# Optimization experiments

Hardware: AMD Instinct MI355X
Metric: run time of the kernel (lower is better)

## Reference

```python
import jax, jax.numpy as jnp
import numpy as np

N = 50000
L = 3


def gcn_conv(x, W, b, src, dst):
    """PyG-style GCNConv: add self-loops, symmetric deg^-1/2 normalization,
    linear transform, scatter-add aggregation at destination nodes."""
    loops = jnp.arange(N, dtype=src.dtype)
    s = jnp.concatenate([src, loops])  # [E+N]
    d = jnp.concatenate([dst, loops])
    deg = jax.ops.segment_sum(jnp.ones(s.shape[0], x.dtype), d, num_segments=N)
    dinv = jnp.where(deg > 0, jax.lax.rsqrt(deg), jnp.zeros_like(deg))
    norm = dinv[s] * dinv[d]  # [E+N]
    xw = x @ W  # [N, F_out]
    out = jax.ops.segment_sum(xw[s] * norm[:, None], d, num_segments=N)
    return out + b


def setup_inputs() -> dict:
    key = jax.random.key(0)
    ks = jax.random.split(key, 6)
    E = 1600000
    F_in, F_hid, F_out = 256, 128, 64
    x = jax.random.normal(ks[0], (N, F_in), dtype=jnp.float32)
    edges = jax.random.randint(ks[1], (L, 2, E), 0, N, dtype=jnp.int32)
    W1 = jax.random.normal(ks[2], (L, F_in, F_hid), dtype=jnp.float32) * (1.0 / np.sqrt(F_in))
    b1 = jnp.zeros((L, F_hid), dtype=jnp.float32)
    W2 = jax.random.normal(ks[3], (L, F_hid, F_out), dtype=jnp.float32) * (1.0 / np.sqrt(F_hid))
    b2 = jnp.zeros((L, F_out), dtype=jnp.float32)
    return {"x": x, "edges": edges, "W1": W1, "b1": b1, "W2": W2, "b2": b2}


def reference(x, edges, W1, b1, W2, b2):
    # layer 1: sum of L GCNConvs over the L rewired graphs
    h = jnp.zeros((N, W1.shape[2]), dtype=x.dtype)
    for i in range(L):
        h = h + gcn_conv(x, W1[i], b1[i], edges[i, 0], edges[i, 1])
    h = jax.nn.relu(h)
    # layer 2
    out = jnp.zeros((N, W2.shape[2]), dtype=x.dtype)
    for i in range(L):
        out = out + gcn_conv(h, W2[i], b2[i], edges[i, 0], edges[i, 1])
    return out
```

## Files before the change

kernel.cpp:

```cpp
#include <hip/hip_runtime.h>

typedef unsigned int uint;
typedef unsigned short ushort;

#define NN 50000
#define NE 1600000
#define NL 3
#define NB 782
#define CAP 2560
#define CHUNK 8192

typedef float f32x4 __attribute__((ext_vector_type(4)));
typedef __bf16 bf16x4v __attribute__((ext_vector_type(4)));
typedef __bf16 bf16x8v __attribute__((ext_vector_type(8)));

__device__ __forceinline__ ushort f2bf(float f) {
    uint u = __float_as_uint(f);
    u += 0x7fffu + ((u >> 16) & 1u);
    return (ushort)(u >> 16);
}
__device__ __forceinline__ float bf2f(uint lo16) { return __uint_as_float(lo16 << 16); }

__global__ void zero_k(int* __restrict__ p, int n) {
    int i = blockIdx.x * 256 + threadIdx.x;
    if (i < n) p[i] = 0;
}

__global__ void cvt_x(const float4* __restrict__ x, ushort4* __restrict__ xb) {
    int idx = blockIdx.x * 256 + threadIdx.x;
    float4 v = x[idx];
    ushort4 o;
    o.x = f2bf(v.x); o.y = f2bf(v.y); o.z = f2bf(v.z); o.w = f2bf(v.w);
    xb[idx] = o;
}

__global__ void cvt_w(const float* __restrict__ W1, const float* __restrict__ W2,
                      ushort* __restrict__ w1t, ushort* __restrict__ w2t) {
    int idx = blockIdx.x * 256 + threadIdx.x;
    const int n1 = NL * 256 * 128;
    const int n2 = NL * 128 * 64;
    if (idx < n1) {
        int i = idx / (128 * 256);
        int rem = idx % (128 * 256);
        int c = rem / 256, k = rem % 256;
        w1t[idx] = f2bf(W1[i * 256 * 128 + k * 128 + c]);
    } else if (idx < n1 + n2) {
        int j = idx - n1;
        int i = j / (64 * 128);
        int rem = j % (64 * 128);
        int c = rem / 128, k = rem % 128;
        w2t[j] = f2bf(W2[i * 128 * 64 + k * 64 + c]);
    }
}

__global__ __launch_bounds__(256) void bin_edges(const int* __restrict__ edges,
                                                 int* __restrict__ gcur,
                                                 uint* __restrict__ bins) {
    __shared__ uint hist[NB];
    __shared__ uint base[NB];
    const int t = threadIdx.x;
    const int g = blockIdx.y;
    const int e0 = blockIdx.x * CHUNK;
    const int n = min(CHUNK, NE - e0);
    const int* srcp = edges + (size_t)g * 2 * NE;
    const int* dstp = srcp + NE;

    for (int b = t; b < NB; b += 256) hist[b] = 0u;
    __syncthreads();
    for (int k = t; k < n; k += 256) {
        int dst = dstp[e0 + k];
        atomicAdd(&hist[dst >> 6], 1u);
    }
    __syncthreads();
    for (int b = t; b < NB; b += 256) {
        uint cnt = hist[b];
        base[b] = cnt ? (uint)atomicAdd(&gcur[g * NB + b], (int)cnt) : 0u;
        hist[b] = 0u;
    }
    __syncthreads();
    for (int k = t; k < n; k += 256) {
        int dst = dstp[e0 + k];
        int src = srcp[e0 + k];
        int b = dst >> 6;
        uint r = atomicAdd(&hist[b], 1u);
        bins[((size_t)g * NB + b) * CAP + base[b] + r] = ((uint)(dst & 63) << 16) | (uint)src;
    }
}

__global__ __launch_bounds__(256) void csr_bucket(const uint* __restrict__ bins,
                                                  const int* __restrict__ gcur,
                                                  uint* __restrict__ rowse,
                                                  float* __restrict__ dinv,
                                                  ushort* __restrict__ colv16) {
    __shared__ uint h[64];
    __shared__ uint off[64];
    const int t = threadIdx.x;
    const int b = blockIdx.x;
    const int g = blockIdx.y;
    if (t < 64) h[t] = 0u;
    __syncthreads();
    const int n = gcur[g * NB + b];
    const uint* pe = bins + ((size_t)g * NB + b) * CAP;
    for (int k = t; k < n; k += 256) atomicAdd(&h[pe[k] >> 16], 1u);
    __syncthreads();
    if (t < 64) {
        uint cnt = h[t];
        uint x = cnt;
#pragma unroll
        for (int o = 1; o < 64; o <<= 1) {
            uint y = __shfl_up(x, o, 64);
            if (t >= o) x += y;
        }
        uint excl = x - cnt;
        off[t] = excl;
        int v = b * 64 + t;
        if (v < NN) {
            rowse[g * NN + v] = (uint)(b * CAP) + excl | (cnt << 24);
            dinv[g * NN + v] = rsqrtf((float)(cnt + 1));
        }
    }
    __syncthreads();
    if (t < 64) h[t] = off[t];
    __syncthreads();
    ushort* cp = colv16 + (size_t)g * NB * CAP + (size_t)b * CAP;
    for (int k = t; k < n; k += 256) {
        uint e = pe[k];
        uint pos = atomicAdd(&h[e >> 16], 1u);
        cp[pos] = (ushort)(e & 0xffffu);
    }
}

template <int KTOT, int BN, bool QUANT>
__global__ __launch_bounds__(256) void gemm_scaled(const ushort* __restrict__ A,
                                                   const ushort* __restrict__ Bt,
                                                   const float* __restrict__ dinv,
                                                   ushort* __restrict__ OutBf,
                                                   char* __restrict__ OutQ,
                                                   float* __restrict__ OutSc, int M) {
    constexpr int LDT = 72;
    constexpr int NREP = BN / 32;
    __shared__ ushort sA[128 * LDT];
    __shared__ ushort sB[BN * LDT];
    __shared__ float pmax[128][2];
    const int t = threadIdx.x;
    const int lane = t & 63;
    const int wid = t >> 6;
    const int wm = wid >> 1, wn = wid & 1;
    const int by = blockIdx.y;
    const int m0 = blockIdx.x * 128;
    const int sr = t >> 3, sc = t & 7;
    const int lr = lane & 15, lg = lane >> 4;

    f32x4 acc[4][NREP];
#pragma unroll
    for (int m = 0; m < 4; ++m)
#pragma unroll
        for (int n = 0; n < NREP; ++n) acc[m][n] = (f32x4){0.f, 0.f, 0.f, 0.f};

    for (int ks = 0; ks < KTOT / 64; ++ks) {
        __syncthreads();
#pragma unroll
        for (int p = 0; p < 4; ++p) {
            int r = sr + p * 32;
            int grow = m0 + r;
            uint4 val = make_uint4(0u, 0u, 0u, 0u);
            if (grow < M)
                val = *reinterpret_cast<const uint4*>(&A[(size_t)grow * KTOT + ks * 64 + sc * 8]);
            *reinterpret_cast<uint4*>(&sA[r * LDT + sc * 8]) = val;
        }
#pragma unroll
        for (int p = 0; p < BN / 32; ++p) {
            int r = sr + p * 32;
            uint4 val =
                *reinterpret_cast<const uint4*>(&Bt[(size_t)(by * BN + r) * KTOT + ks * 64 + sc * 8]);
            *reinterpret_cast<uint4*>(&sB[r * LDT + sc * 8]) = val;
        }
        __syncthreads();
#pragma unroll
        for (int kk = 0; kk < 2; ++kk) {
            const int kb = kk * 32 + lg * 4;
            bf16x8v af[4], bfr[NREP];
#pragma unroll
            for (int m = 0; m < 4; ++m) {
                const __bf16* p =
                    reinterpret_cast<const __bf16*>(&sA[(wm * 64 + m * 16 + lr) * LDT + kb]);
                bf16x4v lo = *reinterpret_cast<const bf16x4v*>(p);
                bf16x4v hi = *reinterpret_cast<const bf16x4v*>(p + 16);
                af[m] = __builtin_shufflevector(lo, hi, 0, 1, 2, 3, 4, 5, 6, 7);
            }
#pragma unroll
            for (int n = 0; n < NREP; ++n) {
                const __bf16* p =
                    reinterpret_cast<const __bf16*>(&sB[(wn * (BN / 2) + n * 16 + lr) * LDT + kb]);
                bf16x4v lo = *reinterpret_cast<const bf16x4v*>(p);
                bf16x4v hi = *reinterpret_cast<const bf16x4v*>(p + 16);
                bfr[n] = __builtin_shufflevector(lo, hi, 0, 1, 2, 3, 4, 5, 6, 7);
            }
#pragma unroll
            for (int m = 0; m < 4; ++m)
#pragma unroll
                for (int n = 0; n < NREP; ++n)
                    acc[m][n] =
                        __builtin_amdgcn_mfma_f32_16x16x32_bf16(af[m], bfr[n], acc[m][n], 0, 0, 0);
        }
    }
    if constexpr (!QUANT) {
#pragma unroll
        for (int m = 0; m < 4; ++m) {
            int rb = m0 + wm * 64 + m * 16 + lg * 4;
#pragma unroll
            for (int n = 0; n < NREP; ++n) {
                int lcol = wn * (BN / 2) + n * 16 + lr;
#pragma unroll
                for (int r = 0; r < 4; ++r) {
                    int grow = rb + r;
                    if (grow < M) {
                        float v = acc[m][n][r] * dinv[by * NN + grow];
                        OutBf[((size_t)by * M + grow) * BN + lcol] = f2bf(v);
                    }
                }
            }
        }
    } else {
        float pm[4][4];
#pragma unroll
        for (int m = 0; m < 4; ++m)
#pragma unroll
            for (int r = 0; r < 4; ++r) {
                float v = fabsf(acc[m][0][r]);
#pragma unroll
                for (int n = 1; n < NREP; ++n) v = fmaxf(v, fabsf(acc[m][n][r]));
#pragma unroll
                for (int o = 1; o < 16; o <<= 1) v = fmaxf(v, __shfl_xor(v, o, 64));
                pm[m][r] = v;
            }
        if (lr == 0) {
#pragma unroll
            for (int m = 0; m < 4; ++m)
#pragma unroll
                for (int r = 0; r < 4; ++r) pmax[wm * 64 + m * 16 + lg * 4 + r][wn] = pm[m][r];
        }
        __syncthreads();
#pragma unroll
        for (int m = 0; m < 4; ++m) {
#pragma unroll
            for (int r = 0; r < 4; ++r) {
                int brow = wm * 64 + m * 16 + lg * 4 + r;
                int grow = m0 + brow;
                if (grow >= M) continue;
                float mx = fmaxf(pmax[brow][0], pmax[brow][1]);
                float rs = (mx > 0.f) ? 127.f / mx : 0.f;
#pragma unroll
                for (int n = 0; n < NREP; ++n) {
                    int q = (int)rintf(acc[m][n][r] * rs);
                    OutQ[((size_t)by * NN + grow) * BN + wn * 64 + n * 16 + lr] = (char)q;
                }
                if (wn == 0 && lr == 0)
                    OutSc[by * NN + grow] =
                        (mx > 0.f) ? mx * dinv[by * NN + grow] * (1.f / 127.f) : 0.f;
            }
        }
    }
}

__global__ __launch_bounds__(256) void agg_l1(const ushort* __restrict__ q1,
                                              const float* __restrict__ q1sc,
                                              const ushort* __restrict__ colv16,
                                              const uint* __restrict__ rowse,
                                              const float* __restrict__ b1,
                                              ushort* __restrict__ hout) {
    const int lane = threadIdx.x & 63;
    const int v = blockIdx.x * 4 + (threadIdx.x >> 6);
    float h0 = 0.f, h1 = 0.f;
#pragma unroll
    for (int i = 0; i < NL; ++i) {
        const ushort* tab = q1 + (size_t)i * NN * 64;
        const float* scp = q1sc + i * NN;
        const ushort* cp = colv16 + (size_t)i * NB * CAP;
        uint se = rowse[i * NN + v];
        int e = (int)(se & 0xffffffu);
        int cnt = (int)(se >> 24);
        const int end = e + cnt;
        float dv = rsqrtf((float)(cnt + 1));
        ushort su = tab[(size_t)v * 64 + lane];
        float ssc = scp[v];
        float a0 = ssc * (float)(char)(su & 0xff);
        float a1 = ssc * (float)(char)(su >> 8);
        for (; e + 8 <= end; e += 8) {
            int s0 = cp[e], s1 = cp[e + 1], s2 = cp[e + 2], s3 = cp[e + 3];
            int s4 = cp[e + 4], s5 = cp[e + 5], s6 = cp[e + 6], s7 = cp[e + 7];
            ushort u0 = tab[(size_t)s0 * 64 + lane];
            ushort u1 = tab[(size_t)s1 * 64 + lane];
            ushort u2 = tab[(size_t)s2 * 64 + lane];
            ushort u3 = tab[(size_t)s3 * 64 + lane];
            ushort u4 = tab[(size_t)s4 * 64 + lane];
            ushort u5 = tab[(size_t)s5 * 64 + lane];
            ushort u6 = tab[(size_t)s6 * 64 + lane];
            ushort u7 = tab[(size_t)s7 * 64 + lane];
            float c0 = scp[s0], c1 = scp[s1], c2 = scp[s2], c3 = scp[s3];
            float c4 = scp[s4], c5 = scp[s5], c6 = scp[s6], c7 = scp[s7];
            a0 = fmaf(c0, (float)(char)(u0 & 0xff), a0); a1 = fmaf(c0, (float)(char)(u0 >> 8), a1);
            a0 = fmaf(c1, (float)(char)(u1 & 0xff), a0); a1 = fmaf(c1, (float)(char)(u1 >> 8), a1);
            a0 = fmaf(c2, (float)(char)(u2 & 0xff), a0); a1 = fmaf(c2, (float)(char)(u2 >> 8), a1);
            a0 = fmaf(c3, (float)(char)(u3 & 0xff), a0); a1 = fmaf(c3, (float)(char)(u3 >> 8), a1);
            a0 = fmaf(c4, (float)(char)(u4 & 0xff), a0); a1 = fmaf(c4, (float)(char)(u4 >> 8), a1);
            a0 = fmaf(c5, (float)(char)(u5 & 0xff), a0); a1 = fmaf(c5, (float)(char)(u5 >> 8), a1);
            a0 = fmaf(c6, (float)(char)(u6 & 0xff), a0); a1 = fmaf(c6, (float)(char)(u6 >> 8), a1);
            a0 = fmaf(c7, (float)(char)(u7 & 0xff), a0); a1 = fmaf(c7, (float)(char)(u7 >> 8), a1);
        }
        for (; e < end; ++e) {
            int s = cp[e];
            ushort u = tab[(size_t)s * 64 + lane];
            float c = scp[s];
            a0 = fmaf(c, (float)(char)(u & 0xff), a0);
            a1 = fmaf(c, (float)(char)(u >> 8), a1);
        }
        h0 = fmaf(dv, a0, h0);
        h1 = fmaf(dv, a1, h1);
    }
    int f0 = lane * 2;
    h0 += b1[f0] + b1[128 + f0] + b1[256 + f0];
    h1 += b1[f0 + 1] + b1[128 + f0 + 1] + b1[256 + f0 + 1];
    h0 = fmaxf(h0, 0.f);
    h1 = fmaxf(h1, 0.f);
    uint o = (uint)f2bf(h0) | ((uint)f2bf(h1) << 16);
    reinterpret_cast<uint*>(hout)[(size_t)v * 64 + lane] = o;
}

__global__ __launch_bounds__(256) void agg_l2(const ushort* __restrict__ hw2s,
                                              const ushort* __restrict__ colv16,
                                              const uint* __restrict__ rowse,
                                              const float* __restrict__ b2,
                                              float* __restrict__ out) {
    const int lane = threadIdx.x & 63;
    const int v = blockIdx.x * 4 + (threadIdx.x >> 6);
    float o = 0.f;
#pragma unroll
    for (int i = 0; i < NL; ++i) {
        const ushort* tab = hw2s + (size_t)i * NN * 64;
        const ushort* cp = colv16 + (size_t)i * NB * CAP;
        uint se = rowse[i * NN + v];
        int e = (int)(se & 0xffffffu);
        int cnt = (int)(se >> 24);
        const int end = e + cnt;
        float dv = rsqrtf((float)(cnt + 1));
        float a = bf2f(tab[(size_t)v * 64 + lane]);
        for (; e + 8 <= end; e += 8) {
            int s0 = cp[e], s1 = cp[e + 1], s2 = cp[e + 2], s3 = cp[e + 3];
            int s4 = cp[e + 4], s5 = cp[e + 5], s6 = cp[e + 6], s7 = cp[e + 7];
            float x0 = bf2f(tab[(size_t)s0 * 64 + lane]);
            float x1 = bf2f(tab[(size_t)s1 * 64 + lane]);
            float x2 = bf2f(tab[(size_t)s2 * 64 + lane]);
            float x3 = bf2f(tab[(size_t)s3 * 64 + lane]);
            float x4 = bf2f(tab[(size_t)s4 * 64 + lane]);
            float x5 = bf2f(tab[(size_t)s5 * 64 + lane]);
            float x6 = bf2f(tab[(size_t)s6 * 64 + lane]);
            float x7 = bf2f(tab[(size_t)s7 * 64 + lane]);
            a += ((x0 + x1) + (x2 + x3)) + ((x4 + x5) + (x6 + x7));
        }
        for (; e < end; ++e) a += bf2f(tab[(size_t)cp[e] * 64 + lane]);
        o = fmaf(dv, a, o);
    }
    o += b2[lane] + b2[64 + lane] + b2[128 + lane];
    out[(size_t)v * 64 + lane] = o;
}

extern "C" void kernel_launch(void* const* d_in, const int* in_sizes, int n_in,
                              void* d_out, int out_size, void* d_ws, size_t ws_size,
                              hipStream_t stream) {
    const float* x = (const float*)d_in[0];
    const int* edges = (const int*)d_in[1];
    const float* W1 = (const float*)d_in[2];
    const float* b1 = (const float*)d_in[3];
    const float* W2 = (const float*)d_in[4];
    const float* b2 = (const float*)d_in[5];
    float* out = (float*)d_out;
    char* ws = (char*)d_ws;

    ushort* xbf    = (ushort*)(ws + 0);
    ushort* w1t    = (ushort*)(ws + 25600000);
    ushort* w2t    = (ushort*)(ws + 25796608);
    uint*   rowse  = (uint*)  (ws + 25845760);
    float*  q1sc   = (float*) (ws + 26445760);
    float*  dinv   = (float*) (ws + 27045760);
    int*    gcur   = (int*)   (ws + 27645760);
    ushort* colv16 = (ushort*)(ws + 27655168);
    uint*   bins   = (uint*)  (ws + 39666688);
    char*   q1     = (char*)  (ws + 63689728);
    ushort* hbf    = (ushort*)(ws + 82889728);
    ushort* hw2s   = (ushort*)(ws + 95689728);

    zero_k<<<dim3((NL * NB + 255) / 256), 256, 0, stream>>>(gcur, NL * NB);
    cvt_x<<<dim3(12500), 256, 0, stream>>>((const float4*)x, (ushort4*)xbf);
    cvt_w<<<dim3(480), 256, 0, stream>>>(W1, W2, w1t, w2t);

    bin_edges<<<dim3((NE + CHUNK - 1) / CHUNK, NL), 256, 0, stream>>>(edges, gcur, bins);
    csr_bucket<<<dim3(NB, NL), 256, 0, stream>>>(bins, gcur, rowse, dinv, colv16);

    gemm_scaled<256, 128, true><<<dim3(391, 3), 256, 0, stream>>>(xbf, w1t, dinv, nullptr, q1,
                                                                  q1sc, NN);
    agg_l1<<<dim3(NN / 4), 256, 0, stream>>>((const ushort*)q1, q1sc, colv16, rowse, b1, hbf);
    gemm_scaled<128, 64, false><<<dim3(391, 3), 256, 0, stream>>>(hbf, w2t, dinv, hw2s, nullptr,
                                                                  nullptr, NN);
    agg_l2<<<dim3(NN / 4), 256, 0, stream>>>(hw2s, colv16, rowse, b2, out);
}
```

Baseline: 435.1 us.

## Fuse fp32-to-bf16 conversion of x into layer-1 GEMM load; nontemporal index loads

Drops the standalone x conversion kernel and converts fp32 x to bf16 inside the first GEMM's shared-memory tile load. This removes a launch and the round trip of the bf16 copy of x through memory. The trade-off is that each of the three column blocks rereads the fp32 x, doubling the bytes per read. The CSR column-index loads in both aggregation kernels now use nontemporal loads to reduce cache pollution.

```diff
diff --git a/kernel.cpp b/kernel.cpp
--- a/kernel.cpp
+++ b/kernel.cpp
@@ -24,14 +24,6 @@
 __global__ void zero_k(int* __restrict__ p, int n) {
     int i = blockIdx.x * 256 + threadIdx.x;
     if (i < n) p[i] = 0;
-}
-
-__global__ void cvt_x(const float4* __restrict__ x, ushort4* __restrict__ xb) {
-    int idx = blockIdx.x * 256 + threadIdx.x;
-    float4 v = x[idx];
-    ushort4 o;
-    o.x = f2bf(v.x); o.y = f2bf(v.y); o.z = f2bf(v.z); o.w = f2bf(v.w);
-    xb[idx] = o;
 }
 
 __global__ void cvt_w(const float* __restrict__ W1, const float* __restrict__ W2,
@@ -130,8 +122,8 @@
     }
 }
 
-template <int KTOT, int BN, bool QUANT>
-__global__ __launch_bounds__(256) void gemm_scaled(const ushort* __restrict__ A,
+template <int KTOT, int BN, bool QUANT, bool F32A>
+__global__ __launch_bounds__(256) void gemm_scaled(const void* __restrict__ Ap,
                                                    const ushort* __restrict__ Bt,
                                                    const float* __restrict__ dinv,
                                                    ushort* __restrict__ OutBf,
@@ -164,8 +156,22 @@
             int r = sr + p * 32;
             int grow = m0 + r;
             uint4 val = make_uint4(0u, 0u, 0u, 0u);
-            if (grow < M)
-                val = *reinterpret_cast<const uint4*>(&A[(size_t)grow * KTOT + ks * 64 + sc * 8]);
+            if (grow < M) {
+                if constexpr (F32A) {
+                    const float* Af = (const float*)Ap;
+                    const float4 lo4 =
+                        *reinterpret_cast<const float4*>(&Af[(size_t)grow * KTOT + ks * 64 + sc * 8]);
+                    const float4 hi4 = *reinterpret_cast<const float4*>(
+                        &Af[(size_t)grow * KTOT + ks * 64 + sc * 8 + 4]);
+                    val.x = (uint)f2bf(lo4.x) | ((uint)f2bf(lo4.y) << 16);
+                    val.y = (uint)f2bf(lo4.z) | ((uint)f2bf(lo4.w) << 16);
+                    val.z = (uint)f2bf(hi4.x) | ((uint)f2bf(hi4.y) << 16);
+                    val.w = (uint)f2bf(hi4.z) | ((uint)f2bf(hi4.w) << 16);
+                } else {
+                    const ushort* Ab = (const ushort*)Ap;
+                    val = *reinterpret_cast<const uint4*>(&Ab[(size_t)grow * KTOT + ks * 64 + sc * 8]);
+                }
+            }
             *reinterpret_cast<uint4*>(&sA[r * LDT + sc * 8]) = val;
         }
 #pragma unroll
@@ -253,7 +259,7 @@
 #pragma unroll
                 for (int n = 0; n < NREP; ++n) {
                     int q = (int)rintf(acc[m][n][r] * rs);
-                    OutQ[((size_t)by * NN + grow) * BN + wn * 64 + n * 16 + lr] = (char)q;
+                    OutQ[((size_t)by * NN + grow) * BN + wn * (BN / 2) + n * 16 + lr] = (char)q;
                 }
                 if (wn == 0 && lr == 0)
                     OutSc[by * NN + grow] =
@@ -287,8 +293,14 @@
         float a0 = ssc * (float)(char)(su & 0xff);
         float a1 = ssc * (float)(char)(su >> 8);
         for (; e + 8 <= end; e += 8) {
-            int s0 = cp[e], s1 = cp[e + 1], s2 = cp[e + 2], s3 = cp[e + 3];
-            int s4 = cp[e + 4], s5 = cp[e + 5], s6 = cp[e + 6], s7 = cp[e + 7];
+            int s0 = __builtin_nontemporal_load(&cp[e]);
+            int s1 = __builtin_nontemporal_load(&cp[e + 1]);
+            int s2 = __builtin_nontemporal_load(&cp[e + 2]);
+            int s3 = __builtin_nontemporal_load(&cp[e + 3]);
+            int s4 = __builtin_nontemporal_load(&cp[e + 4]);
+            int s5 = __builtin_nontemporal_load(&cp[e + 5]);
+            int s6 = __builtin_nontemporal_load(&cp[e + 6]);
+            int s7 = __builtin_nontemporal_load(&cp[e + 7]);
             ushort u0 = tab[(size_t)s0 * 64 + lane];
             ushort u1 = tab[(size_t)s1 * 64 + lane];
             ushort u2 = tab[(size_t)s2 * 64 + lane];
@@ -309,7 +321,7 @@
             a0 = fmaf(c7, (float)(char)(u7 & 0xff), a0); a1 = fmaf(c7, (float)(char)(u7 >> 8), a1);
         }
         for (; e < end; ++e) {
-            int s = cp[e];
+            int s = __builtin_nontemporal_load(&cp[e]);
             ushort u = tab[(size_t)s * 64 + lane];
             float c = scp[s];
             a0 = fmaf(c, (float)(char)(u & 0xff), a0);
@@ -346,8 +358,14 @@
         float dv = rsqrtf((float)(cnt + 1));
         float a = bf2f(tab[(size_t)v * 64 + lane]);
         for (; e + 8 <= end; e += 8) {
-            int s0 = cp[e], s1 = cp[e + 1], s2 = cp[e + 2], s3 = cp[e + 3];
-            int s4 = cp[e + 4], s5 = cp[e + 5], s6 = cp[e + 6], s7 = cp[e + 7];
+            int s0 = __builtin_nontemporal_load(&cp[e]);
+            int s1 = __builtin_nontemporal_load(&cp[e + 1]);
+            int s2 = __builtin_nontemporal_load(&cp[e + 2]);
+            int s3 = __builtin_nontemporal_load(&cp[e + 3]);
+            int s4 = __builtin_nontemporal_load(&cp[e + 4]);
+            int s5 = __builtin_nontemporal_load(&cp[e + 5]);
+            int s6 = __builtin_nontemporal_load(&cp[e + 6]);
+            int s7 = __builtin_nontemporal_load(&cp[e + 7]);
             float x0 = bf2f(tab[(size_t)s0 * 64 + lane]);
             float x1 = bf2f(tab[(size_t)s1 * 64 + lane]);
             float x2 = bf2f(tab[(size_t)s2 * 64 + lane]);
@@ -358,7 +376,10 @@
             float x7 = bf2f(tab[(size_t)s7 * 64 + lane]);
             a += ((x0 + x1) + (x2 + x3)) + ((x4 + x5) + (x6 + x7));
         }
-        for (; e < end; ++e) a += bf2f(tab[(size_t)cp[e] * 64 + lane]);
+        for (; e < end; ++e) {
+            int s = __builtin_nontemporal_load(&cp[e]);
+            a += bf2f(tab[(size_t)s * 64 + lane]);
+        }
         o = fmaf(dv, a, o);
     }
     o += b2[lane] + b2[64 + lane] + b2[128 + lane];
@@ -377,30 +398,28 @@
     float* out = (float*)d_out;
     char* ws = (char*)d_ws;
 
-    ushort* xbf    = (ushort*)(ws + 0);
-    ushort* w1t    = (ushort*)(ws + 25600000);
-    ushort* w2t    = (ushort*)(ws + 25796608);
-    uint*   rowse  = (uint*)  (ws + 25845760);
-    float*  q1sc   = (float*) (ws + 26445760);
-    float*  dinv   = (float*) (ws + 27045760);
-    int*    gcur   = (int*)   (ws + 27645760);
-    ushort* colv16 = (ushort*)(ws + 27655168);
-    uint*   bins   = (uint*)  (ws + 39666688);
-    char*   q1     = (char*)  (ws + 63689728);
-    ushort* hbf    = (ushort*)(ws + 82889728);
-    ushort* hw2s   = (ushort*)(ws + 95689728);
+    ushort* w1t    = (ushort*)(ws + 0);
+    ushort* w2t    = (ushort*)(ws + 196608);
+    uint*   rowse  = (uint*)  (ws + 245760);
+    float*  q1sc   = (float*) (ws + 845760);
+    float*  dinv   = (float*) (ws + 1445760);
+    int*    gcur   = (int*)   (ws + 2045760);
+    ushort* colv16 = (ushort*)(ws + 2055168);
+    uint*   bins   = (uint*)  (ws + 14066688);
+    char*   q1     = (char*)  (ws + 38089728);
+    ushort* hbf    = (ushort*)(ws + 57289728);
+    ushort* hw2s   = (ushort*)(ws + 70089728);
 
     zero_k<<<dim3((NL * NB + 255) / 256), 256, 0, stream>>>(gcur, NL * NB);
-    cvt_x<<<dim3(12500), 256, 0, stream>>>((const float4*)x, (ushort4*)xbf);
     cvt_w<<<dim3(480), 256, 0, stream>>>(W1, W2, w1t, w2t);
 
     bin_edges<<<dim3((NE + CHUNK - 1) / CHUNK, NL), 256, 0, stream>>>(edges, gcur, bins);
     csr_bucket<<<dim3(NB, NL), 256, 0, stream>>>(bins, gcur, rowse, dinv, colv16);
 
-    gemm_scaled<256, 128, true><<<dim3(391, 3), 256, 0, stream>>>(xbf, w1t, dinv, nullptr, q1,
-                                                                  q1sc, NN);
+    gemm_scaled<256, 128, true, true><<<dim3(391, 3), 256, 0, stream>>>(x, w1t, dinv, nullptr,
+                                                                        q1, q1sc, NN);
     agg_l1<<<dim3(NN / 4), 256, 0, stream>>>((const ushort*)q1, q1sc, colv16, rowse, b1, hbf);
-    gemm_scaled<128, 64, false><<<dim3(391, 3), 256, 0, stream>>>(hbf, w2t, dinv, hw2s, nullptr,
-                                                                  nullptr, NN);
+    gemm_scaled<128, 64, false, false><<<dim3(391, 3), 256, 0, stream>>>(hbf, w2t, dinv, hw2s,
+                                                                         nullptr, nullptr, NN);
     agg_l2<<<dim3(NN / 4), 256, 0, stream>>>(hw2s, colv16, rowse, b2, out);
 }
```

Result: slower. 496.1 us (+14.0%).
